# Kernel tuning notes

Measured on AMD Instinct MI355X. Metric: run time of the kernel, lower is better.

## Reference

```python
import jax, jax.numpy as jnp
import numpy as np

B, D, N = 256, 256, 100000
NUM_CLUSTERS, NUM_CLASSES = 100, 1000


def setup_inputs() -> dict:
    key = jax.random.key(0)
    k1, k2, k3, k4, k5, k6 = jax.random.split(key, 6)
    return {
        "feature": jax.random.normal(k1, (B, D), dtype=jnp.float32),
        "feature_bank": jax.random.normal(k2, (N, D), dtype=jnp.float32),
        "cluster_label_bank": jax.random.randint(k3, (N,), 0, NUM_CLUSTERS, dtype=jnp.int64)
            if jax.config.jax_enable_x64 else jax.random.randint(k3, (N,), 0, NUM_CLUSTERS).astype(jnp.int32),
        "class_label_bank": jax.random.randint(k4, (N,), 0, NUM_CLASSES).astype(jnp.int32),
        "cluster_idx": jax.random.randint(k5, (B,), 0, NUM_CLUSTERS).astype(jnp.int32),
        "gt_label": jax.random.randint(k6, (B,), 0, NUM_CLASSES).astype(jnp.int32),
    }


def reference(feature, feature_bank, cluster_label_bank, class_label_bank, cluster_idx, gt_label):
    # Masks: primary = same cluster AND different class; fallback = different class only.
    cluster_label_bank = cluster_label_bank.astype(jnp.int32)
    same_cluster = cluster_label_bank[None, :] == cluster_idx[:, None].astype(jnp.int32)  # [B, N]
    diff_class = class_label_bank[None, :] != gt_label[:, None]                            # [B, N]
    mask_primary = same_cluster & diff_class
    has_primary = mask_primary.any(axis=1, keepdims=True)
    mask = jnp.where(has_primary, mask_primary, diff_class)  # [B, N]

    # Euclidean distances (torch.cdist p=2): ||a-b|| via expanded squared form.
    a2 = jnp.sum(feature * feature, axis=1)[:, None]              # [B, 1]
    b2 = jnp.sum(feature_bank * feature_bank, axis=1)[None, :]    # [1, N]
    d2 = a2 + b2 - 2.0 * (feature @ feature_bank.T)               # [B, N]
    dist = jnp.sqrt(jnp.maximum(d2, 0.0))

    # Masked argmin over the bank, then gather negatives.
    dist_masked = jnp.where(mask, dist, jnp.inf)
    neg_idx = jnp.argmin(dist_masked, axis=1)                     # [B]
    negatives = feature_bank[neg_idx]                             # [B, D]
    return negatives
```

## Files before the change

kernel.cpp:

```cpp
#include <hip/hip_runtime.h>
#include <climits>

typedef __attribute__((ext_vector_type(8))) short s8;
typedef __attribute__((ext_vector_type(4))) float f32x4;

#define BQ    256
#define DDIM  256
#define NBANK 100000
#define BN    64
#define NJB   ((NBANK + BN - 1) / BN)
#define SENT  1e30f

__device__ inline void splitElem(float x, s8& h, s8& l, int i) {
    unsigned u  = __float_as_uint(x);
    unsigned uh = (u + 0x8000u) & 0xFFFF0000u;
    h[i] = (short)(uh >> 16);
    float lf = x - __uint_as_float(uh);
    l[i] = (short)((__float_as_uint(lf) + 0x8000u) >> 16);
}

__device__ inline void split8(const float4 v0, const float4 v1, s8& h, s8& l) {
    splitElem(v0.x, h, l, 0); splitElem(v0.y, h, l, 1);
    splitElem(v0.z, h, l, 2); splitElem(v0.w, h, l, 3);
    splitElem(v1.x, h, l, 4); splitElem(v1.y, h, l, 5);
    splitElem(v1.z, h, l, 6); splitElem(v1.w, h, l, 7);
}

__device__ inline float sq8(const float4 v0, const float4 v1, float s) {
    s = fmaf(v0.x, v0.x, s); s = fmaf(v0.y, v0.y, s);
    s = fmaf(v0.z, v0.z, s); s = fmaf(v0.w, v0.w, s);
    s = fmaf(v1.x, v1.x, s); s = fmaf(v1.y, v1.y, s);
    s = fmaf(v1.z, v1.z, s); s = fmaf(v1.w, v1.w, s);
    return s;
}

__global__ __launch_bounds__(512) void split_feature(
    const float* __restrict__ feature, s8* __restrict__ fH, s8* __restrict__ fL)
{
    const int t    = blockIdx.x * 512 + threadIdx.x;
    const int lane = t & 63, ks = (t >> 6) & 7, rt = t >> 9;
    const int row  = rt * 16 + (lane & 15);
    const int k0   = ks * 32 + (lane >> 4) * 8;
    const float* p = feature + (size_t)row * DDIM + k0;
    const float4 v0 = *(const float4*)p;
    const float4 v1 = *(const float4*)(p + 4);
    s8 h, l;
    split8(v0, v1, h, l);
    fH[t] = h; fL[t] = l;
}

__global__ __launch_bounds__(256, 3) void gemm_argmin_partial(
    const s8* __restrict__ fH, const s8* __restrict__ fL,
    const float* __restrict__ bank,
    const int* __restrict__ cluster_label, const int* __restrict__ class_label,
    const int* __restrict__ cluster_idx,  const int* __restrict__ gt_label,
    float* __restrict__ wsPV, int* __restrict__ wsPI,
    float* __restrict__ wsDV, int* __restrict__ wsDI)
{
    __shared__ __align__(16) s8 bHs[4 * 64];
    __shared__ __align__(16) s8 bLs[4 * 64];
    __shared__ float b2s[BN];
    __shared__ int clsS[BN], cluS[BN], rowGt[BQ], rowClu[BQ];

    const int tid = threadIdx.x;
    const int jb  = blockIdx.x;
    const int j0  = jb * BN;

    if (tid < BN) {
        int jg = j0 + tid;
        int jc = jg < NBANK ? jg : NBANK - 1;
        clsS[tid] = class_label[jc];
        cluS[tid] = cluster_label[jc];
    }
    rowGt[tid]  = gt_label[tid];
    rowClu[tid] = cluster_idx[tid];

    const int col = tid >> 2, q = tid & 3;
    const int ct_s = col >> 4, cl_s = col & 15;
    const int wi   = ct_s * 64 + q * 16 + cl_s;
    {
        int jcol = j0 + col;
        jcol = jcol < NBANK ? jcol : NBANK - 1;
        const float* gb = bank + (size_t)jcol * DDIM + q * 8;

        const int w = tid >> 6, lane = tid & 63;
        const int g = lane >> 4, c = lane & 15;

        f32x4 acc[4][4];
        #pragma unroll
        for (int ct = 0; ct < 4; ++ct)
            #pragma unroll
            for (int rt = 0; rt < 4; ++rt)
                acc[ct][rt] = (f32x4){0.f, 0.f, 0.f, 0.f};
        float sqa = 0.f;

        float4 cur0 = *(const float4*)(gb);
        float4 cur1 = *(const float4*)(gb + 4);

        for (int s = 0; s < 8; ++s) {
            s8 aHr[4], aLr[4];
            #pragma unroll
            for (int rt = 0; rt < 4; ++rt) {
                const int RT = w * 4 + rt;
                aHr[rt] = fH[(RT * 8 + s) * 64 + lane];
                aLr[rt] = fL[(RT * 8 + s) * 64 + lane];
            }
            __syncthreads();
            {
                s8 h, l;
                split8(cur0, cur1, h, l);
                sqa = sq8(cur0, cur1, sqa);
                bHs[wi] = h;
                bLs[wi] = l;
            }
            __syncthreads();
            if (s < 7) {
                cur0 = *(const float4*)(gb + (s + 1) * 32);
                cur1 = *(const float4*)(gb + (s + 1) * 32 + 4);
            }
            #pragma unroll
            for (int ct = 0; ct < 4; ++ct) {
                const s8 bh = bHs[ct * 64 + lane];
                const s8 bl = bLs[ct * 64 + lane];
                #pragma unroll
                for (int rt = 0; rt < 4; ++rt) {
                    acc[ct][rt] = __builtin_amdgcn_mfma_f32_16x16x32_bf16(aHr[rt], bh, acc[ct][rt], 0, 0, 0);
                    acc[ct][rt] = __builtin_amdgcn_mfma_f32_16x16x32_bf16(aHr[rt], bl, acc[ct][rt], 0, 0, 0);
                    acc[ct][rt] = __builtin_amdgcn_mfma_f32_16x16x32_bf16(aLr[rt], bh, acc[ct][rt], 0, 0, 0);
                    acc[ct][rt] = __builtin_amdgcn_mfma_f32_16x16x32_bf16(aLr[rt], bl, acc[ct][rt], 0, 0, 0);
                }
            }
        }

        sqa += __shfl_xor(sqa, 1);
        sqa += __shfl_xor(sqa, 2);
        if (q == 0) b2s[col] = sqa;
        __syncthreads();

        #pragma unroll
        for (int rt = 0; rt < 4; ++rt) {
            #pragma unroll
            for (int r = 0; r < 4; ++r) {
                const int row  = w * 64 + rt * 16 + g * 4 + r;
                const int myGt = rowGt[row], myClu = rowClu[row];
                float bpv = SENT, bdv = SENT;
                int   bpi = INT_MAX, bdi = INT_MAX;
                #pragma unroll
                for (int ct = 0; ct < 4; ++ct) {
                    const int jg = j0 + ct * 16 + c;
                    const float sc = b2s[ct * 16 + c] - 2.f * acc[ct][rt][r];
                    if (jg < NBANK && clsS[ct * 16 + c] != myGt) {
                        if (sc < bdv) { bdv = sc; bdi = jg; }
                        if (cluS[ct * 16 + c] == myClu && sc < bpv) { bpv = sc; bpi = jg; }
                    }
                }
                #pragma unroll
                for (int off = 1; off < 16; off <<= 1) {
                    float vv = __shfl_xor(bpv, off); int ii = __shfl_xor(bpi, off);
                    if (vv < bpv || (vv == bpv && ii < bpi)) { bpv = vv; bpi = ii; }
                    vv = __shfl_xor(bdv, off); ii = __shfl_xor(bdi, off);
                    if (vv < bdv || (vv == bdv && ii < bdi)) { bdv = vv; bdi = ii; }
                }
                if (c == 0) {
                    const size_t o = (size_t)row * NJB + jb;
                    wsPV[o] = bpv; wsPI[o] = bpi;
                    wsDV[o] = bdv; wsDI[o] = bdi;
                }
            }
        }
    }
}

__global__ __launch_bounds__(256) void reduce_gather(
    const float* __restrict__ wsPV, const int* __restrict__ wsPI,
    const float* __restrict__ wsDV, const int* __restrict__ wsDI,
    const float* __restrict__ bank, float* __restrict__ out)
{
    const int row = blockIdx.x, tid = threadIdx.x;
    float bpv = SENT, bdv = SENT;
    int   bpi = INT_MAX, bdi = INT_MAX;
    for (int b = tid; b < NJB; b += 256) {
        float v = wsPV[(size_t)row * NJB + b]; int ix = wsPI[(size_t)row * NJB + b];
        if (v < bpv || (v == bpv && ix < bpi)) { bpv = v; bpi = ix; }
        v = wsDV[(size_t)row * NJB + b]; ix = wsDI[(size_t)row * NJB + b];
        if (v < bdv || (v == bdv && ix < bdi)) { bdv = v; bdi = ix; }
    }
    #pragma unroll
    for (int off = 32; off > 0; off >>= 1) {
        float v = __shfl_down(bpv, off); int ix = __shfl_down(bpi, off);
        if (v < bpv || (v == bpv && ix < bpi)) { bpv = v; bpi = ix; }
        v = __shfl_down(bdv, off); ix = __shfl_down(bdi, off);
        if (v < bdv || (v == bdv && ix < bdi)) { bdv = v; bdi = ix; }
    }
    __shared__ float swPV[4], swDV[4];
    __shared__ int   swPI[4], swDI[4];
    __shared__ int   sIdx;
    const int lane = tid & 63, wv = tid >> 6;
    if (lane == 0) { swPV[wv] = bpv; swPI[wv] = bpi; swDV[wv] = bdv; swDI[wv] = bdi; }
    __syncthreads();
    if (tid == 0) {
        float pv = swPV[0]; int pi = swPI[0];
        float dv = swDV[0]; int di = swDI[0];
        #pragma unroll
        for (int w = 1; w < 4; ++w) {
            if (swPV[w] < pv || (swPV[w] == pv && swPI[w] < pi)) { pv = swPV[w]; pi = swPI[w]; }
            if (swDV[w] < dv || (swDV[w] == dv && swDI[w] < di)) { dv = swDV[w]; di = swDI[w]; }
        }
        sIdx = (pi != INT_MAX) ? pi : ((di != INT_MAX) ? di : 0);
    }
    __syncthreads();
    out[row * DDIM + tid] = bank[(size_t)sIdx * DDIM + tid];
}

extern "C" void kernel_launch(void* const* d_in, const int* in_sizes, int n_in,
                              void* d_out, int out_size, void* d_ws, size_t ws_size,
                              hipStream_t stream) {
    const float* feature       = (const float*)d_in[0];
    const float* bank          = (const float*)d_in[1];
    const int*   cluster_label = (const int*)d_in[2];
    const int*   class_label   = (const int*)d_in[3];
    const int*   cluster_idx   = (const int*)d_in[4];
    const int*   gt_label      = (const int*)d_in[5];
    float* out = (float*)d_out;

    s8* fH = (s8*)d_ws;
    s8* fL = fH + 8192;
    float* base = (float*)((char*)d_ws + 2 * 8192 * sizeof(s8));
    const size_t per = (size_t)BQ * NJB;
    float* wsPV = base;
    int*   wsPI = (int*)base + per;
    float* wsDV = base + 2 * per;
    int*   wsDI = (int*)base + 3 * per;

    hipLaunchKernelGGL(split_feature, dim3(16), dim3(512), 0, stream, feature, fH, fL);
    hipLaunchKernelGGL(gemm_argmin_partial, dim3(NJB), dim3(256), 0, stream,
                       fH, fL, bank, cluster_label, class_label, cluster_idx, gt_label,
                       wsPV, wsPI, wsDV, wsDI);
    hipLaunchKernelGGL(reduce_gather, dim3(BQ), dim3(256), 0, stream,
                       wsPV, wsPI, wsDV, wsDI, bank, out);
}
```

Measured before the change: 239.9 us.

## Replace per-block argmin partials with packed 64-bit atomicMin and restructure GEMM staging

Each bank tile's argmin candidate is now packed as an order-preserving float+index 64-bit key and merged into per-row global slots with atomicMin, guarded by a volatile pre-read. This removes the large partial-result workspace and the full reduction pass, leaving only a small gather kernel. The GEMM kernel also loads the whole 64x256 bank tile up front, splits it into shared memory once with a single barrier, and double-buffers the A-fragment loads. The larger shared staging and register use lower occupancy (launch bound 3 to 2), and atomic contention on the 512 slots is a risk.

Result: slower. 341.8 us (+42.5%).

```diff
diff --git a/kernel.cpp b/kernel.cpp
--- a/kernel.cpp
+++ b/kernel.cpp
@@ -10,6 +10,7 @@
 #define BN    64
 #define NJB   ((NBANK + BN - 1) / BN)
 #define SENT  1e30f
+#define INIT64 0xFFFFFFFFFFFFFFFFULL
 
 __device__ inline void splitElem(float x, s8& h, s8& l, int i) {
     unsigned u  = __float_as_uint(x);
@@ -34,9 +35,20 @@
     return s;
 }
 
-__global__ __launch_bounds__(512) void split_feature(
-    const float* __restrict__ feature, s8* __restrict__ fH, s8* __restrict__ fL)
+__device__ inline unsigned long long packMin(float v, int idx) {
+    unsigned b = __float_as_uint(v);
+    unsigned u = (b & 0x80000000u) ? ~b : (b | 0x80000000u);
+    return ((unsigned long long)u << 32) | (unsigned)idx;
+}
+
+__global__ __launch_bounds__(512) void prep(
+    const float* __restrict__ feature, s8* __restrict__ fH, s8* __restrict__ fL,
+    unsigned long long* __restrict__ slots)
 {
+    if (blockIdx.x == 16) {
+        slots[threadIdx.x] = INIT64;
+        return;
+    }
     const int t    = blockIdx.x * 512 + threadIdx.x;
     const int lane = t & 63, ks = (t >> 6) & 7, rt = t >> 9;
     const int row  = rt * 16 + (lane & 15);
@@ -49,16 +61,15 @@
     fH[t] = h; fL[t] = l;
 }
 
-__global__ __launch_bounds__(256, 3) void gemm_argmin_partial(
+__global__ __launch_bounds__(256, 2) void gemm_argmin(
     const s8* __restrict__ fH, const s8* __restrict__ fL,
     const float* __restrict__ bank,
     const int* __restrict__ cluster_label, const int* __restrict__ class_label,
     const int* __restrict__ cluster_idx,  const int* __restrict__ gt_label,
-    float* __restrict__ wsPV, int* __restrict__ wsPI,
-    float* __restrict__ wsDV, int* __restrict__ wsDI)
+    unsigned long long* __restrict__ slots)
 {
-    __shared__ __align__(16) s8 bHs[4 * 64];
-    __shared__ __align__(16) s8 bLs[4 * 64];
+    __shared__ __align__(16) s8 bHs[8 * 4 * 64];
+    __shared__ __align__(16) s8 bLs[8 * 4 * 64];
     __shared__ float b2s[BN];
     __shared__ int clsS[BN], cluS[BN], rowGt[BQ], rowClu[BQ];
 
@@ -76,140 +87,130 @@
     rowClu[tid] = cluster_idx[tid];
 
     const int col = tid >> 2, q = tid & 3;
-    const int ct_s = col >> 4, cl_s = col & 15;
-    const int wi   = ct_s * 64 + q * 16 + cl_s;
     {
         int jcol = j0 + col;
         jcol = jcol < NBANK ? jcol : NBANK - 1;
         const float* gb = bank + (size_t)jcol * DDIM + q * 8;
-
-        const int w = tid >> 6, lane = tid & 63;
-        const int g = lane >> 4, c = lane & 15;
-
-        f32x4 acc[4][4];
-        #pragma unroll
-        for (int ct = 0; ct < 4; ++ct)
-            #pragma unroll
-            for (int rt = 0; rt < 4; ++rt)
-                acc[ct][rt] = (f32x4){0.f, 0.f, 0.f, 0.f};
+        float4 v[8][2];
+        #pragma unroll
+        for (int s = 0; s < 8; ++s) {
+            v[s][0] = *(const float4*)(gb + s * 32);
+            v[s][1] = *(const float4*)(gb + s * 32 + 4);
+        }
+        const int ct_s = col >> 4, cl_s = col & 15;
+        const int wi   = ct_s * 64 + q * 16 + cl_s;
         float sqa = 0.f;
-
-        float4 cur0 = *(const float4*)(gb);
-        float4 cur1 = *(const float4*)(gb + 4);
-
+        #pragma unroll
         for (int s = 0; s < 8; ++s) {
-            s8 aHr[4], aLr[4];
-            #pragma unroll
-            for (int rt = 0; rt < 4; ++rt) {
-                const int RT = w * 4 + rt;
-                aHr[rt] = fH[(RT * 8 + s) * 64 + lane];
-                aLr[rt] = fL[(RT * 8 + s) * 64 + lane];
-            }
-            __syncthreads();
-            {
-                s8 h, l;
-                split8(cur0, cur1, h, l);
-                sqa = sq8(cur0, cur1, sqa);
-                bHs[wi] = h;
-                bLs[wi] = l;
-            }
-            __syncthreads();
-            if (s < 7) {
-                cur0 = *(const float4*)(gb + (s + 1) * 32);
-                cur1 = *(const float4*)(gb + (s + 1) * 32 + 4);
-            }
-            #pragma unroll
-            for (int ct = 0; ct < 4; ++ct) {
-                const s8 bh = bHs[ct * 64 + lane];
-                const s8 bl = bLs[ct * 64 + lane];
-                #pragma unroll
-                for (int rt = 0; rt < 4; ++rt) {
-                    acc[ct][rt] = __builtin_amdgcn_mfma_f32_16x16x32_bf16(aHr[rt], bh, acc[ct][rt], 0, 0, 0);
-                    acc[ct][rt] = __builtin_amdgcn_mfma_f32_16x16x32_bf16(aHr[rt], bl, acc[ct][rt], 0, 0, 0);
-                    acc[ct][rt] = __builtin_amdgcn_mfma_f32_16x16x32_bf16(aLr[rt], bh, acc[ct][rt], 0, 0, 0);
-                    acc[ct][rt] = __builtin_amdgcn_mfma_f32_16x16x32_bf16(aLr[rt], bl, acc[ct][rt], 0, 0, 0);
-                }
-            }
-        }
-
+            s8 h, l;
+            split8(v[s][0], v[s][1], h, l);
+            sqa = sq8(v[s][0], v[s][1], sqa);
+            bHs[s * 256 + wi] = h;
+            bLs[s * 256 + wi] = l;
+        }
         sqa += __shfl_xor(sqa, 1);
         sqa += __shfl_xor(sqa, 2);
         if (q == 0) b2s[col] = sqa;
-        __syncthreads();
-
-        #pragma unroll
-        for (int rt = 0; rt < 4; ++rt) {
-            #pragma unroll
-            for (int r = 0; r < 4; ++r) {
-                const int row  = w * 64 + rt * 16 + g * 4 + r;
-                const int myGt = rowGt[row], myClu = rowClu[row];
-                float bpv = SENT, bdv = SENT;
-                int   bpi = INT_MAX, bdi = INT_MAX;
-                #pragma unroll
-                for (int ct = 0; ct < 4; ++ct) {
-                    const int jg = j0 + ct * 16 + c;
-                    const float sc = b2s[ct * 16 + c] - 2.f * acc[ct][rt][r];
-                    if (jg < NBANK && clsS[ct * 16 + c] != myGt) {
-                        if (sc < bdv) { bdv = sc; bdi = jg; }
-                        if (cluS[ct * 16 + c] == myClu && sc < bpv) { bpv = sc; bpi = jg; }
-                    }
+    }
+    __syncthreads();
+
+    const int w = tid >> 6, lane = tid & 63;
+    const int g = lane >> 4, c = lane & 15;
+
+    f32x4 acc[4][4];
+    #pragma unroll
+    for (int ct = 0; ct < 4; ++ct)
+        #pragma unroll
+        for (int rt = 0; rt < 4; ++rt)
+            acc[ct][rt] = (f32x4){0.f, 0.f, 0.f, 0.f};
+
+    s8 aH[4], aL[4], nH[4], nL[4];
+    #pragma unroll
+    for (int rt = 0; rt < 4; ++rt) {
+        aH[rt] = fH[((w * 4 + rt) * 8 + 0) * 64 + lane];
+        aL[rt] = fL[((w * 4 + rt) * 8 + 0) * 64 + lane];
+    }
+    #pragma unroll
+    for (int s = 0; s < 8; ++s) {
+        if (s < 7) {
+            #pragma unroll
+            for (int rt = 0; rt < 4; ++rt) {
+                nH[rt] = fH[((w * 4 + rt) * 8 + s + 1) * 64 + lane];
+                nL[rt] = fL[((w * 4 + rt) * 8 + s + 1) * 64 + lane];
+            }
+        }
+        #pragma unroll
+        for (int ct = 0; ct < 4; ++ct) {
+            const s8 bh = bHs[s * 256 + ct * 64 + lane];
+            const s8 bl = bLs[s * 256 + ct * 64 + lane];
+            #pragma unroll
+            for (int rt = 0; rt < 4; ++rt) {
+                acc[ct][rt] = __builtin_amdgcn_mfma_f32_16x16x32_bf16(aH[rt], bh, acc[ct][rt], 0, 0, 0);
+                acc[ct][rt] = __builtin_amdgcn_mfma_f32_16x16x32_bf16(aH[rt], bl, acc[ct][rt], 0, 0, 0);
+                acc[ct][rt] = __builtin_amdgcn_mfma_f32_16x16x32_bf16(aL[rt], bh, acc[ct][rt], 0, 0, 0);
+                acc[ct][rt] = __builtin_amdgcn_mfma_f32_16x16x32_bf16(aL[rt], bl, acc[ct][rt], 0, 0, 0);
+            }
+        }
+        #pragma unroll
+        for (int rt = 0; rt < 4; ++rt) { aH[rt] = nH[rt]; aL[rt] = nL[rt]; }
+    }
+
+    #pragma unroll
+    for (int rt = 0; rt < 4; ++rt) {
+        #pragma unroll
+        for (int r = 0; r < 4; ++r) {
+            const int row  = w * 64 + rt * 16 + g * 4 + r;
+            const int myGt = rowGt[row], myClu = rowClu[row];
+            float bpv = SENT, bdv = SENT;
+            int   bpi = INT_MAX, bdi = INT_MAX;
+            #pragma unroll
+            for (int ct = 0; ct < 4; ++ct) {
+                const int jg = j0 + ct * 16 + c;
+                const float sc = b2s[ct * 16 + c] - 2.f * acc[ct][rt][r];
+                if (jg < NBANK && clsS[ct * 16 + c] != myGt) {
+                    if (sc < bdv) { bdv = sc; bdi = jg; }
+                    if (cluS[ct * 16 + c] == myClu && sc < bpv) { bpv = sc; bpi = jg; }
                 }
-                #pragma unroll
-                for (int off = 1; off < 16; off <<= 1) {
-                    float vv = __shfl_xor(bpv, off); int ii = __shfl_xor(bpi, off);
-                    if (vv < bpv || (vv == bpv && ii < bpi)) { bpv = vv; bpi = ii; }
-                    vv = __shfl_xor(bdv, off); ii = __shfl_xor(bdi, off);
-                    if (vv < bdv || (vv == bdv && ii < bdi)) { bdv = vv; bdi = ii; }
+            }
+            #pragma unroll
+            for (int off = 1; off < 16; off <<= 1) {
+                float vv = __shfl_xor(bpv, off); int ii = __shfl_xor(bpi, off);
+                if (vv < bpv || (vv == bpv && ii < bpi)) { bpv = vv; bpi = ii; }
+                vv = __shfl_xor(bdv, off); ii = __shfl_xor(bdi, off);
+                if (vv < bdv || (vv == bdv && ii < bdi)) { bdv = vv; bdi = ii; }
+            }
+            if (c == 0) {
+                if (bpi != INT_MAX) {
+                    const unsigned long long pk = packMin(bpv, bpi);
+                    const unsigned long long cur =
+                        *(const volatile unsigned long long*)(slots + row);
+                    if (pk < cur) atomicMin(slots + row, pk);
                 }
-                if (c == 0) {
-                    const size_t o = (size_t)row * NJB + jb;
-                    wsPV[o] = bpv; wsPI[o] = bpi;
-                    wsDV[o] = bdv; wsDI[o] = bdi;
+                if (bdi != INT_MAX) {
+                    const unsigned long long pk = packMin(bdv, bdi);
+                    const unsigned long long cur =
+                        *(const volatile unsigned long long*)(slots + 256 + row);
+                    if (pk < cur) atomicMin(slots + 256 + row, pk);
                 }
             }
         }
     }
 }
 
-__global__ __launch_bounds__(256) void reduce_gather(
-    const float* __restrict__ wsPV, const int* __restrict__ wsPI,
-    const float* __restrict__ wsDV, const int* __restrict__ wsDI,
+__global__ __launch_bounds__(256) void gather(
+    const unsigned long long* __restrict__ slots,
     const float* __restrict__ bank, float* __restrict__ out)
 {
-    const int row = blockIdx.x, tid = threadIdx.x;
-    float bpv = SENT, bdv = SENT;
-    int   bpi = INT_MAX, bdi = INT_MAX;
-    for (int b = tid; b < NJB; b += 256) {
-        float v = wsPV[(size_t)row * NJB + b]; int ix = wsPI[(size_t)row * NJB + b];
-        if (v < bpv || (v == bpv && ix < bpi)) { bpv = v; bpi = ix; }
-        v = wsDV[(size_t)row * NJB + b]; ix = wsDI[(size_t)row * NJB + b];
-        if (v < bdv || (v == bdv && ix < bdi)) { bdv = v; bdi = ix; }
-    }
-    #pragma unroll
-    for (int off = 32; off > 0; off >>= 1) {
-        float v = __shfl_down(bpv, off); int ix = __shfl_down(bpi, off);
-        if (v < bpv || (v == bpv && ix < bpi)) { bpv = v; bpi = ix; }
-        v = __shfl_down(bdv, off); ix = __shfl_down(bdi, off);
-        if (v < bdv || (v == bdv && ix < bdi)) { bdv = v; bdi = ix; }
-    }
-    __shared__ float swPV[4], swDV[4];
-    __shared__ int   swPI[4], swDI[4];
-    __shared__ int   sIdx;
-    const int lane = tid & 63, wv = tid >> 6;
-    if (lane == 0) { swPV[wv] = bpv; swPI[wv] = bpi; swDV[wv] = bdv; swDI[wv] = bdi; }
+    const int row = blockIdx.x, t = threadIdx.x;
+    __shared__ int sIdx;
+    if (t == 0) {
+        unsigned long long p = slots[row];
+        unsigned long long d = slots[256 + row];
+        unsigned long long chosen = (p != INIT64) ? p : d;
+        sIdx = (chosen != INIT64) ? (int)(unsigned)(chosen & 0xFFFFFFFFu) : 0;
+    }
     __syncthreads();
-    if (tid == 0) {
-        float pv = swPV[0]; int pi = swPI[0];
-        float dv = swDV[0]; int di = swDI[0];
-        #pragma unroll
-        for (int w = 1; w < 4; ++w) {
-            if (swPV[w] < pv || (swPV[w] == pv && swPI[w] < pi)) { pv = swPV[w]; pi = swPI[w]; }
-            if (swDV[w] < dv || (swDV[w] == dv && swDI[w] < di)) { dv = swDV[w]; di = swDI[w]; }
-        }
-        sIdx = (pi != INT_MAX) ? pi : ((di != INT_MAX) ? di : 0);
-    }
-    __syncthreads();
-    out[row * DDIM + tid] = bank[(size_t)sIdx * DDIM + tid];
+    out[row * DDIM + t] = bank[(size_t)sIdx * DDIM + t];
 }
 
 extern "C" void kernel_launch(void* const* d_in, const int* in_sizes, int n_in,
@@ -225,17 +226,11 @@
 
     s8* fH = (s8*)d_ws;
     s8* fL = fH + 8192;
-    float* base = (float*)((char*)d_ws + 2 * 8192 * sizeof(s8));
-    const size_t per = (size_t)BQ * NJB;
-    float* wsPV = base;
-    int*   wsPI = (int*)base + per;
-    float* wsDV = base + 2 * per;
-    int*   wsDI = (int*)base + 3 * per;
-
-    hipLaunchKernelGGL(split_feature, dim3(16), dim3(512), 0, stream, feature, fH, fL);
-    hipLaunchKernelGGL(gemm_argmin_partial, dim3(NJB), dim3(256), 0, stream,
+    unsigned long long* slots = (unsigned long long*)(fL + 8192);
+
+    hipLaunchKernelGGL(prep, dim3(17), dim3(512), 0, stream, feature, fH, fL, slots);
+    hipLaunchKernelGGL(gemm_argmin, dim3(NJB), dim3(256), 0, stream,
                        fH, fL, bank, cluster_label, class_label, cluster_idx, gt_label,
-                       wsPV, wsPI, wsDV, wsDI);
-    hipLaunchKernelGGL(reduce_gather, dim3(BQ), dim3(256), 0, stream,
-                       wsPV, wsPI, wsDV, wsDI, bank, out);
-}
+                       slots);
+    hipLaunchKernelGGL(gather, dim3(BQ), dim3(256), 0, stream, slots, bank, out);
+}
```
